# Kernel tuning notes

Measured on AMD Instinct MI355X. Metric: run time of the kernel, lower is better.

The kernel has to match this reference:

```python
import jax, jax.numpy as jnp
import numpy as np
from jax import lax

KERNEL_EPS = 1e-4   # eps in softmax_kernel
ATTN_EPS = 1e-6     # eps in causal_linear_attention
CHUNK = 64          # chunk length for the causal scan


def softmax_kernel(data, projection_matrix, is_query):
    # data: [b,h,n,d], projection_matrix: [r,d]
    d = data.shape[-1]
    r = projection_matrix.shape[0]
    data_normalizer = d ** -0.25
    ratio = r ** -0.5
    data_dash = jnp.einsum('bhnd,rd->bhnr', data_normalizer * data, projection_matrix)
    diag_data = (jnp.sum(data ** 2, axis=-1) * 0.5 * data_normalizer ** 2)[..., None]  # [b,h,n,1]
    if is_query:
        stab = jnp.max(data_dash, axis=-1, keepdims=True)
    else:
        stab = jnp.max(data_dash)
    return ratio * (jnp.exp(data_dash - diag_data - stab) + KERNEL_EPS)


def causal_linear_attention(qp, kp, v, chunk=CHUNK, eps=ATTN_EPS):
    # qp,kp: [b,h,n,r] feature maps; v: [b,h,n,e]
    b, h, n, r = qp.shape
    e = v.shape[-1]
    nc = n // chunk
    # -> [nc, b, h, chunk, *] for lax.scan over chunks
    qs = jnp.moveaxis(qp.reshape(b, h, nc, chunk, r), 2, 0)
    ks = jnp.moveaxis(kp.reshape(b, h, nc, chunk, r), 2, 0)
    vs = jnp.moveaxis(v.reshape(b, h, nc, chunk, e), 2, 0)

    def step(carry, xs):
        k_last, ctx_last = carry  # [b,h,r], [b,h,r,e]
        qch, kch, vch = xs        # [b,h,c,r], [b,h,c,r], [b,h,c,e]
        k_cum = k_last[:, :, None, :] + jnp.cumsum(kch, axis=2)              # [b,h,c,r]
        D_inv = 1.0 / jnp.einsum('bhcr,bhcr->bhc', qch, k_cum + eps)         # [b,h,c]
        ctx = jnp.einsum('bhcr,bhce->bhcre', kch, vch)                       # [b,h,c,r,e]
        ctx_cum = ctx_last[:, :, None] + jnp.cumsum(ctx, axis=2)             # [b,h,c,r,e]
        out = jnp.einsum('bhcre,bhcr,bhc->bhce', ctx_cum, qch, D_inv)        # [b,h,c,e]
        return (k_cum[:, :, -1], ctx_cum[:, :, -1]), out

    init = (jnp.zeros((b, h, r), qp.dtype), jnp.zeros((b, h, r, e), qp.dtype))
    _, outs = lax.scan(step, init, (qs, ks, vs))  # outs: [nc,b,h,c,e]
    return jnp.moveaxis(outs, 0, 2).reshape(b, h, n, e)


def setup_inputs() -> dict:
    key = jax.random.key(0)
    kq, kk, kv, kp = jax.random.split(key, 4)
    b, h, n, d, r = 2, 8, 4096, 64, 256
    q = jax.random.normal(kq, (b, h, n, d), dtype=jnp.float32)
    k = jax.random.normal(kk, (b, h, n, d), dtype=jnp.float32)
    v = jax.random.normal(kv, (b, h, n, d), dtype=jnp.float32)
    projection_matrix = jax.random.normal(kp, (r, d), dtype=jnp.float32)
    return {"q": q, "k": k, "v": v, "projection_matrix": projection_matrix}


def reference(q, k, v, projection_matrix):
    qp = softmax_kernel(q, projection_matrix, is_query=True)
    kp = softmax_kernel(k, projection_matrix, is_query=False)
    return causal_linear_attention(qp, kp, v)
```

## Files before the change

### kernel.cpp

```cpp
#include <hip/hip_runtime.h>


typedef unsigned short ushort_t;
typedef __attribute__((ext_vector_type(8))) short bf16x8;
typedef __attribute__((ext_vector_type(4))) float f32x4;

#define KEPS 1e-4f
#define AEPS 1e-6f
#define NORMIZER 0.35355339059327373f
#define RATIO 0.0625f

__device__ __forceinline__ ushort_t bf16r(float f) {
  unsigned u = __float_as_uint(f);
  return (ushort_t)((u + 0x7fffu + ((u >> 16) & 1u)) >> 16);
}
__device__ __forceinline__ float ubf(ushort_t h) {
  return __uint_as_float((unsigned)h << 16);
}

__global__ __launch_bounds__(256) void pconv_kernel(
    const float* __restrict__ P, ushort_t* __restrict__ Phi,
    ushort_t* __restrict__ Plo)
{
  int idx = blockIdx.x * 1024 + threadIdx.x;
  #pragma unroll
  for (int p = 0; p < 4; ++p) {
    int i = idx + p * 256;
    float x = P[i];
    ushort_t h = bf16r(x);
    Phi[i] = h;
    Plo[i] = bf16r(x - ubf(h));
  }
}

__global__ __launch_bounds__(256, 4) void feat_mfma(
    const float* __restrict__ Q, const float* __restrict__ K,
    const ushort_t* __restrict__ Phi, const ushort_t* __restrict__ Plo,
    ushort_t* __restrict__ qp, ushort_t* __restrict__ E,
    float* __restrict__ bmax)
{
  __shared__ union {
    struct { ushort_t Xhi[64 * 72]; ushort_t Xlo[64 * 72]; } s;
    ushort_t outb[64 * 72];
  } u;
  __shared__ ushort_t Pq[2][64 * 72];
  __shared__ float diagS[64];
  __shared__ float redm[4];

  int bid = blockIdx.x, tid = threadIdx.x;
  bool isK = bid >= 1024;
  const float* X = isK ? K : Q;
  size_t rowbase = (size_t)(isK ? bid - 1024 : bid) * 64;

  #pragma unroll
  for (int p = 0; p < 4; ++p) {
    int idx = tid + p * 256;
    int row = idx >> 4, c4 = idx & 15;
    float4 x = *(const float4*)&X[(rowbase + row) * 64 + c4 * 4];
    ushort4 h, l;
    h.x = bf16r(x.x); l.x = bf16r(x.x - ubf(h.x));
    h.y = bf16r(x.y); l.y = bf16r(x.y - ubf(h.y));
    h.z = bf16r(x.z); l.z = bf16r(x.z - ubf(h.z));
    h.w = bf16r(x.w); l.w = bf16r(x.w - ubf(h.w));
    *(ushort4*)&u.s.Xhi[row * 72 + c4 * 4] = h;
    *(ushort4*)&u.s.Xlo[row * 72 + c4 * 4] = l;
    float ss = x.x * x.x + x.y * x.y + x.z * x.z + x.w * x.w;
    ss += __shfl_xor(ss, 1, 64); ss += __shfl_xor(ss, 2, 64);
    ss += __shfl_xor(ss, 4, 64); ss += __shfl_xor(ss, 8, 64);
    if ((tid & 15) == 0) diagS[row] = 0.0625f * ss;
  }
  __syncthreads();

  int lane = tid & 63, wv = tid >> 6;
  int n15 = lane & 15, quad = lane >> 4;

  bf16x8 ah[2], al[2];
  #pragma unroll
  for (int ks = 0; ks < 2; ++ks) {
    int off = (16 * wv + n15) * 72 + quad * 8 + 32 * ks;
    ah[ks] = *(const bf16x8*)&u.s.Xhi[off];
    al[ks] = *(const bf16x8*)&u.s.Xlo[off];
  }

  f32x4 acc[16];
  #pragma unroll
  for (int tc = 0; tc < 16; ++tc) acc[tc] = f32x4{0.f, 0.f, 0.f, 0.f};

  #pragma unroll
  for (int q4 = 0; q4 < 4; ++q4) {
    if (q4) __syncthreads();
    #pragma unroll
    for (int t = 0; t < 2; ++t) {
      int f = tid + t * 256;
      int cl = f >> 3, k8 = (f & 7) * 8;
      size_t g = (size_t)(q4 * 64 + cl) * 64 + k8;
      *(bf16x8*)&Pq[0][cl * 72 + k8] = *(const bf16x8*)&Phi[g];
      *(bf16x8*)&Pq[1][cl * 72 + k8] = *(const bf16x8*)&Plo[g];
    }
    __syncthreads();
    #pragma unroll
    for (int tcl = 0; tcl < 4; ++tcl) {
      f32x4 a = acc[q4 * 4 + tcl];
      #pragma unroll
      for (int ks = 0; ks < 2; ++ks) {
        int off = (16 * tcl + n15) * 72 + quad * 8 + 32 * ks;
        bf16x8 bh = *(const bf16x8*)&Pq[0][off];
        bf16x8 bl = *(const bf16x8*)&Pq[1][off];
        a = __builtin_amdgcn_mfma_f32_16x16x32_bf16(ah[ks], bh, a, 0, 0, 0);
        a = __builtin_amdgcn_mfma_f32_16x16x32_bf16(ah[ks], bl, a, 0, 0, 0);
        a = __builtin_amdgcn_mfma_f32_16x16x32_bf16(al[ks], bh, a, 0, 0, 0);
      }
      acc[q4 * 4 + tcl] = a;
    }
  }

  float dg[4];
  #pragma unroll
  for (int r = 0; r < 4; ++r) dg[r] = diagS[16 * wv + quad * 4 + r];

  float sub[4];
  if (!isK) {
    #pragma unroll
    for (int r = 0; r < 4; ++r) {
      float mx = -3.0e38f;
      #pragma unroll
      for (int tc = 0; tc < 16; ++tc) mx = fmaxf(mx, acc[tc][r]);
      #pragma unroll
      for (int s = 1; s < 16; s <<= 1) mx = fmaxf(mx, __shfl_xor(mx, s, 64));
      sub[r] = dg[r] + NORMIZER * mx;
    }
  } else {
    float bm = -3.0e38f;
    #pragma unroll
    for (int tc = 0; tc < 16; ++tc)
      #pragma unroll
      for (int r = 0; r < 4; ++r) bm = fmaxf(bm, acc[tc][r]);
    #pragma unroll
    for (int s = 1; s < 64; s <<= 1) bm = fmaxf(bm, __shfl_xor(bm, s, 64));
    if (lane == 0) redm[wv] = bm;
    #pragma unroll
    for (int r = 0; r < 4; ++r) sub[r] = dg[r];
  }

  ushort_t* dst = (isK ? E : qp) + rowbase * 256;
  #pragma unroll
  for (int qt = 0; qt < 4; ++qt) {
    __syncthreads();
    #pragma unroll
    for (int t4 = 0; t4 < 4; ++t4) {
      int tc = qt * 4 + t4;
      #pragma unroll
      for (int r = 0; r < 4; ++r) {
        int row = 16 * wv + quad * 4 + r;
        float ex = __expf(NORMIZER * acc[tc][r] - sub[r]);
        float val = isK ? ex : RATIO * (ex + KEPS);
        u.outb[row * 72 + t4 * 16 + n15] = bf16r(val);
      }
    }
    __syncthreads();
    int row = tid >> 2, c0 = (tid & 3) * 16;
    bf16x8 v0 = *(const bf16x8*)&u.outb[row * 72 + c0];
    bf16x8 v1 = *(const bf16x8*)&u.outb[row * 72 + c0 + 8];
    *(bf16x8*)&dst[row * 256 + qt * 64 + c0] = v0;
    *(bf16x8*)&dst[row * 256 + qt * 64 + c0 + 8] = v1;
  }

  if (isK && tid == 0) {
    float m4 = fmaxf(fmaxf(redm[0], redm[1]), fmaxf(redm[2], redm[3]));
    bmax[bid - 1024] = NORMIZER * m4;
  }
}

__global__ __launch_bounds__(256) void kmax_reduce(
    const float* __restrict__ bmax, float* __restrict__ kmax)
{
  __shared__ float red[4];
  int tid = threadIdx.x;
  float m = fmaxf(fmaxf(bmax[tid], bmax[tid + 256]),
                  fmaxf(bmax[tid + 512], bmax[tid + 768]));
  #pragma unroll
  for (int s = 1; s < 64; s <<= 1) m = fmaxf(m, __shfl_xor(m, s, 64));
  if ((tid & 63) == 0) red[tid >> 6] = m;
  __syncthreads();
  if (tid == 0)
    *kmax = fmaxf(fmaxf(red[0], red[1]), fmaxf(red[2], red[3]));
}

__global__ __launch_bounds__(256) void chunksum_mfma(
    const ushort_t* __restrict__ E, const float* __restrict__ V,
    ushort_t* __restrict__ SE, float* __restrict__ zE, float* __restrict__ SV)
{
  __shared__ ushort_t Et[256 * 72];
  __shared__ ushort_t Vt[64 * 72];
  __shared__ float red2[256];

  int bc = blockIdx.x, tid = threadIdx.x;
  size_t ebase = (size_t)bc * 16384;

  #pragma unroll
  for (int p = 0; p < 8; ++p) {
    int g = (tid + p * 256) * 8;
    int pos = g >> 8, j0 = g & 255;
    bf16x8 ev = *(const bf16x8*)&E[ebase + g];
    #pragma unroll
    for (int jj = 0; jj < 8; ++jj) {
      int j = j0 + jj;
      int pr = (pos + 8 * ((j >> 3) & 7)) & 63;
      Et[j * 72 + pr] = (ushort_t)ev[jj];
    }
  }
  float vsum = 0.f;
  #pragma unroll
  for (int p = 0; p < 16; ++p) {
    int g = tid + p * 256;
    int pos = g >> 6, e = g & 63;
    float x = V[(size_t)bc * 4096 + g];
    vsum += x;
    int pr = (pos + 8 * ((e >> 3) & 7)) & 63;
    Vt[e * 72 + pr] = bf16r(x);
  }
  red2[tid] = vsum;
  __syncthreads();
  if (tid < 64)
    SV[(size_t)bc * 64 + tid] =
        red2[tid] + red2[64 + tid] + red2[128 + tid] + red2[192 + tid];

  {
    float s = 0.f;
    #pragma unroll
    for (int m8 = 0; m8 < 8; ++m8) {
      bf16x8 r8 = *(const bf16x8*)&Et[tid * 72 + m8 * 8];
      #pragma unroll
      for (int x = 0; x < 8; ++x) s += ubf((ushort_t)r8[x]);
    }
    zE[(size_t)bc * 256 + tid] = s;
  }

  int lane = tid & 63, wv = tid >> 6;
  int n15 = lane & 15, quad = lane >> 4;

  bf16x8 aV[2];
  {
    int e = 16 * wv + n15;
    int rot = 8 * ((e >> 3) & 7);
    #pragma unroll
    for (int ks = 0; ks < 2; ++ks) {
      int pr = (quad * 8 + 32 * ks + rot) & 63;
      aV[ks] = *(const bf16x8*)&Vt[e * 72 + pr];
    }
  }

  f32x4 acc[16];
  #pragma unroll
  for (int tc = 0; tc < 16; ++tc) {
    int j = 16 * tc + n15;
    int rot = 8 * ((j >> 3) & 7);
    f32x4 a = {0.f, 0.f, 0.f, 0.f};
    #pragma unroll
    for (int ks = 0; ks < 2; ++ks) {
      int pr = (quad * 8 + 32 * ks + rot) & 63;
      bf16x8 b = *(const bf16x8*)&Et[j * 72 + pr];
      a = __builtin_amdgcn_mfma_f32_16x16x32_bf16(aV[ks], b, a, 0, 0, 0);
    }
    acc[tc] = a;
  }
  __syncthreads();

  ushort_t* outS = Et;
  #pragma unroll
  for (int tc = 0; tc < 16; ++tc)
    #pragma unroll
    for (int r = 0; r < 4; ++r) {
      int e = 16 * wv + quad * 4 + r;
      outS[e * 264 + 16 * tc + n15] = bf16r(acc[tc][r]);
    }
  __syncthreads();
  #pragma unroll
  for (int p = 0; p < 8; ++p) {
    int g = (tid + p * 256) * 8;
    int e = g >> 8, j0 = g & 255;
    bf16x8 vv = *(const bf16x8*)&outS[e * 264 + j0];
    *(bf16x8*)&SE[ebase + g] = vv;
  }
}

__global__ __launch_bounds__(256) void prefix_kernel(
    ushort_t* __restrict__ S, float* __restrict__ zE,
    const float* __restrict__ SV, const float* __restrict__ kmax)
{
  int b = blockIdx.x;
  float m = *kmax;
  float c1 = RATIO * __expf(-m);
  const float c0 = RATIO * KEPS;
  if (b < 1024) {
    int flat = b * 256 + threadIdx.x;
    int bh = flat >> 14;
    int idx = flat & 16383;
    int e = idx >> 8;
    size_t base = (size_t)bh * 1048576 + idx;
    const float* svp = SV + (size_t)bh * 4096 + e;
    float runE = 0.f, runV = 0.f;
    for (int cc = 0; cc < 64; cc += 8) {
      ushort_t t[8]; float sv[8];
      #pragma unroll
      for (int u2 = 0; u2 < 8; ++u2) {
        t[u2] = S[base + (size_t)(cc + u2) * 16384];
        sv[u2] = svp[(size_t)(cc + u2) * 64];
      }
      #pragma unroll
      for (int u2 = 0; u2 < 8; ++u2) {
        S[base + (size_t)(cc + u2) * 16384] = bf16r(c1 * runE + c0 * runV);
        runE += ubf(t[u2]);
        runV += sv[u2];
      }
    }
  } else {
    int bh = b - 1024;
    int j = threadIdx.x;
    size_t base = (size_t)bh * 16384 + j;
    float run = 0.f;
    for (int cc = 0; cc < 64; cc += 8) {
      float t[8];
      #pragma unroll
      for (int u2 = 0; u2 < 8; ++u2)
        t[u2] = zE[base + (size_t)(cc + u2) * 256];
      #pragma unroll
      for (int u2 = 0; u2 < 8; ++u2) {
        zE[base + (size_t)(cc + u2) * 256] = run;
        run += c1 * t[u2] + 64.0f * c0;
      }
    }
  }
}

__global__ __launch_bounds__(256) void fused_mfma(
    const ushort_t* __restrict__ qp, const ushort_t* __restrict__ E,
    const float* __restrict__ kmax, const float* __restrict__ Z,
    const ushort_t* __restrict__ S, const float* __restrict__ V,
    float* __restrict__ out)
{
  __shared__ ushort_t As[64 * 72];
  __shared__ ushort_t Vt[64 * 72];
  __shared__ float zv[256];
  __shared__ float qsumS[64];
  __shared__ float dqS[64];

  int bc = blockIdx.x, tid = threadIdx.x;
  int lane = tid & 63, wv = tid >> 6;
  int n15 = lane & 15, quad = lane >> 4;
  float m = *kmax;
  float c1 = RATIO * __expf(-m);
  const float c0 = RATIO * KEPS;
  size_t base = (size_t)bc * 16384;

  zv[tid] = Z[(size_t)bc * 256 + tid] + AEPS;
  #pragma unroll
  for (int p = 0; p < 16; ++p) {
    int idx = tid + p * 256;
    int t = idx >> 6, e = idx & 63;
    Vt[e * 72 + t] = bf16r(V[(size_t)bc * 4096 + idx]);
  }
  __syncthreads();

  bf16x8 aQ[8];
  #pragma unroll
  for (int ks = 0; ks < 8; ++ks)
    aQ[ks] = *(const bf16x8*)&qp[base + (size_t)(16 * wv + n15) * 256 + quad * 8 + 32 * ks];

  float qsum = 0.f, dq = 0.f;
  #pragma unroll
  for (int ks = 0; ks < 8; ++ks)
    #pragma unroll
    for (int j = 0; j < 8; ++j) {
      float qv = ubf((ushort_t)aQ[ks][j]);
      qsum += qv;
      dq += qv * zv[quad * 8 + 32 * ks + j];
    }
  qsum += __shfl_xor(qsum, 16, 64); qsum += __shfl_xor(qsum, 32, 64);
  dq   += __shfl_xor(dq, 16, 64);   dq   += __shfl_xor(dq, 32, 64);
  if (quad == 0) { qsumS[16 * wv + n15] = qsum; dqS[16 * wv + n15] = dq; }

  bf16x8 bcur[8], bnxt[8];
  #pragma unroll
  for (int ks = 0; ks < 8; ++ks)
    bcur[ks] = *(const bf16x8*)&E[base + (size_t)n15 * 256 + quad * 8 + 32 * ks];

  float rs[4] = {0.f, 0.f, 0.f, 0.f};
  #pragma unroll
  for (int tc = 0; tc < 4; ++tc) {
    if (tc < 3) {
      #pragma unroll
      for (int ks = 0; ks < 8; ++ks)
        bnxt[ks] = *(const bf16x8*)&E[base + (size_t)(16 * (tc + 1) + n15) * 256 + quad * 8 + 32 * ks];
    }
    f32x4 g = {0.f, 0.f, 0.f, 0.f};
    #pragma unroll
    for (int ks = 0; ks < 8; ++ks)
      g = __builtin_amdgcn_mfma_f32_16x16x32_bf16(aQ[ks], bcur[ks], g, 0, 0, 0);
    #pragma unroll
    for (int r = 0; r < 4; ++r) {
      int i = 16 * wv + quad * 4 + r;
      int t = 16 * tc + n15;
      float val = (t <= i) ? (c1 * g[r] + c0 * qsumS[i]) : 0.f;
      As[i * 72 + t] = bf16r(val);
      rs[r] += val;
    }
    #pragma unroll
    for (int ks = 0; ks < 8; ++ks) bcur[ks] = bnxt[ks];
  }

  float dinv[4];
  #pragma unroll
  for (int r = 0; r < 4; ++r) {
    float v = rs[r];
    #pragma unroll
    for (int s = 1; s < 16; s <<= 1) v += __shfl_xor(v, s, 64);
    int i = 16 * wv + quad * 4 + r;
    dinv[r] = 1.f / (dqS[i] + v);
  }

  #pragma unroll
  for (int ks = 0; ks < 8; ++ks)
    bcur[ks] = *(const bf16x8*)&S[base + (size_t)n15 * 256 + quad * 8 + 32 * ks];

  #pragma unroll
  for (int ec = 0; ec < 4; ++ec) {
    if (ec < 3) {
      #pragma unroll
      for (int ks = 0; ks < 8; ++ks)
        bnxt[ks] = *(const bf16x8*)&S[base + (size_t)(16 * (ec + 1) + n15) * 256 + quad * 8 + 32 * ks];
    }
    f32x4 o = {0.f, 0.f, 0.f, 0.f};
    #pragma unroll
    for (int ks = 0; ks < 8; ++ks)
      o = __builtin_amdgcn_mfma_f32_16x16x32_bf16(aQ[ks], bcur[ks], o, 0, 0, 0);
    #pragma unroll
    for (int ks = 0; ks < 2; ++ks) {
      bf16x8 a2 = *(const bf16x8*)&As[(16 * wv + n15) * 72 + quad * 8 + 32 * ks];
      bf16x8 b2 = *(const bf16x8*)&Vt[(16 * ec + n15) * 72 + quad * 8 + 32 * ks];
      o = __builtin_amdgcn_mfma_f32_16x16x32_bf16(a2, b2, o, 0, 0, 0);
    }
    #pragma unroll
    for (int r = 0; r < 4; ++r) {
      int i = 16 * wv + quad * 4 + r;
      out[(size_t)bc * 4096 + (size_t)i * 64 + 16 * ec + n15] = o[r] * dinv[r];
    }
    #pragma unroll
    for (int ks = 0; ks < 8; ++ks) bcur[ks] = bnxt[ks];
  }
}

extern "C" void kernel_launch(void* const* d_in, const int* in_sizes, int n_in,
                              void* d_out, int out_size, void* d_ws, size_t ws_size,
                              hipStream_t stream)
{
  const float* q = (const float*)d_in[0];
  const float* k = (const float*)d_in[1];
  const float* v = (const float*)d_in[2];
  const float* P = (const float*)d_in[3];
  float* out = (float*)d_out;

  ushort_t* qp  = (ushort_t*)d_ws;
  ushort_t* E   = qp + 16777216;
  ushort_t* S   = E + 16777216;
  float*    zE  = (float*)(S + 16777216);
  float*    SV  = zE + 262144;
  ushort_t* Phi = (ushort_t*)(SV + 65536);
  ushort_t* Plo = Phi + 16384;
  float*    bmax = (float*)(Plo + 16384);
  float*    kmax = bmax + 1024;

  pconv_kernel<<<16, 256, 0, stream>>>(P, Phi, Plo);
  feat_mfma<<<2048, 256, 0, stream>>>(q, k, Phi, Plo, qp, E, bmax);
  kmax_reduce<<<1, 256, 0, stream>>>(bmax, kmax);
  chunksum_mfma<<<1024, 256, 0, stream>>>(E, v, S, zE, SV);
  prefix_kernel<<<1040, 256, 0, stream>>>(S, zE, SV, kmax);
  fused_mfma<<<1024, 256, 0, stream>>>(qp, E, kmax, zE, S, v, out);
}
```

Baseline: 185.3 us.

## Stage E/S tiles into swizzled LDS via async global_load_lds double buffering

In the fused chunk kernel, each wave used to load the shared E and S tiles straight from global memory into registers, so all four waves read the same data separately. Now each 16-row tile is loaded once per block with global_load_lds into a double-buffered LDS area, using an XOR swizzle to avoid bank conflicts. The E and S phases are merged into one 8-step loop that prefetches the next tile while the current one runs through MFMA. This cuts redundant global traffic and register pressure, but adds a barrier and vmcnt wait every step.

```diff
diff --git a/kernel.cpp b/kernel.cpp
--- a/kernel.cpp
+++ b/kernel.cpp
@@ -333,6 +333,20 @@
   }
 }
 
+__device__ __forceinline__ void stage_tile(const ushort_t* __restrict__ gt,
+                                           ushort_t* lds0, int tid, int wv) {
+  #pragma unroll
+  for (int i = 0; i < 2; ++i) {
+    int D = i * 256 + tid;
+    int row = D >> 5, cl = D & 31;
+    int sc = (row << 5) | (cl ^ (row & 7));
+    __builtin_amdgcn_global_load_lds(
+        (const __attribute__((address_space(1))) void*)(gt + sc * 8),
+        (__attribute__((address_space(3))) void*)(lds0 + (i * 256 + wv * 64) * 8),
+        16, 0, 0);
+  }
+}
+
 __global__ __launch_bounds__(256) void fused_mfma(
     const ushort_t* __restrict__ qp, const ushort_t* __restrict__ E,
     const float* __restrict__ kmax, const float* __restrict__ Z,
@@ -341,6 +355,7 @@
 {
   __shared__ ushort_t As[64 * 72];
   __shared__ ushort_t Vt[64 * 72];
+  __shared__ ushort_t Bst[2][4096];
   __shared__ float zv[256];
   __shared__ float qsumS[64];
   __shared__ float dqS[64];
@@ -362,6 +377,8 @@
   }
   __syncthreads();
 
+  stage_tile(E + base, &Bst[0][0], tid, wv);
+
   bf16x8 aQ[8];
   #pragma unroll
   for (int ks = 0; ks < 8; ++ks)
@@ -380,73 +397,65 @@
   dq   += __shfl_xor(dq, 16, 64);   dq   += __shfl_xor(dq, 32, 64);
   if (quad == 0) { qsumS[16 * wv + n15] = qsum; dqS[16 * wv + n15] = dq; }
 
-  bf16x8 bcur[8], bnxt[8];
-  #pragma unroll
-  for (int ks = 0; ks < 8; ++ks)
-    bcur[ks] = *(const bf16x8*)&E[base + (size_t)n15 * 256 + quad * 8 + 32 * ks];
-
   float rs[4] = {0.f, 0.f, 0.f, 0.f};
-  #pragma unroll
-  for (int tc = 0; tc < 4; ++tc) {
-    if (tc < 3) {
-      #pragma unroll
-      for (int ks = 0; ks < 8; ++ks)
-        bnxt[ks] = *(const bf16x8*)&E[base + (size_t)(16 * (tc + 1) + n15) * 256 + quad * 8 + 32 * ks];
+  float dinv[4] = {0.f, 0.f, 0.f, 0.f};
+
+  #pragma unroll
+  for (int t = 0; t < 8; ++t) {
+    asm volatile("s_waitcnt vmcnt(0)" ::: "memory");
+    __builtin_amdgcn_s_barrier();
+    if (t < 7) {
+      const ushort_t* gt = (t < 3) ? (E + base + (size_t)(t + 1) * 4096)
+                                   : (S + base + (size_t)(t - 3) * 4096);
+      stage_tile(gt, &Bst[(t + 1) & 1][0], tid, wv);
+    }
+
+    bf16x8 bf[8];
+    #pragma unroll
+    for (int ks = 0; ks < 8; ++ks) {
+      int rc = (4 * ks + quad) ^ (n15 & 7);
+      bf[ks] = *(const bf16x8*)&Bst[t & 1][(n15 * 32 + rc) * 8];
     }
     f32x4 g = {0.f, 0.f, 0.f, 0.f};
     #pragma unroll
     for (int ks = 0; ks < 8; ++ks)
-      g = __builtin_amdgcn_mfma_f32_16x16x32_bf16(aQ[ks], bcur[ks], g, 0, 0, 0);
-    #pragma unroll
-    for (int r = 0; r < 4; ++r) {
-      int i = 16 * wv + quad * 4 + r;
-      int t = 16 * tc + n15;
-      float val = (t <= i) ? (c1 * g[r] + c0 * qsumS[i]) : 0.f;
-      As[i * 72 + t] = bf16r(val);
-      rs[r] += val;
-    }
-    #pragma unroll
-    for (int ks = 0; ks < 8; ++ks) bcur[ks] = bnxt[ks];
-  }
-
-  float dinv[4];
-  #pragma unroll
-  for (int r = 0; r < 4; ++r) {
-    float v = rs[r];
-    #pragma unroll
-    for (int s = 1; s < 16; s <<= 1) v += __shfl_xor(v, s, 64);
-    int i = 16 * wv + quad * 4 + r;
-    dinv[r] = 1.f / (dqS[i] + v);
-  }
-
-  #pragma unroll
-  for (int ks = 0; ks < 8; ++ks)
-    bcur[ks] = *(const bf16x8*)&S[base + (size_t)n15 * 256 + quad * 8 + 32 * ks];
-
-  #pragma unroll
-  for (int ec = 0; ec < 4; ++ec) {
-    if (ec < 3) {
-      #pragma unroll
-      for (int ks = 0; ks < 8; ++ks)
-        bnxt[ks] = *(const bf16x8*)&S[base + (size_t)(16 * (ec + 1) + n15) * 256 + quad * 8 + 32 * ks];
-    }
-    f32x4 o = {0.f, 0.f, 0.f, 0.f};
-    #pragma unroll
-    for (int ks = 0; ks < 8; ++ks)
-      o = __builtin_amdgcn_mfma_f32_16x16x32_bf16(aQ[ks], bcur[ks], o, 0, 0, 0);
-    #pragma unroll
-    for (int ks = 0; ks < 2; ++ks) {
-      bf16x8 a2 = *(const bf16x8*)&As[(16 * wv + n15) * 72 + quad * 8 + 32 * ks];
-      bf16x8 b2 = *(const bf16x8*)&Vt[(16 * ec + n15) * 72 + quad * 8 + 32 * ks];
-      o = __builtin_amdgcn_mfma_f32_16x16x32_bf16(a2, b2, o, 0, 0, 0);
-    }
-    #pragma unroll
-    for (int r = 0; r < 4; ++r) {
-      int i = 16 * wv + quad * 4 + r;
-      out[(size_t)bc * 4096 + (size_t)i * 64 + 16 * ec + n15] = o[r] * dinv[r];
-    }
-    #pragma unroll
-    for (int ks = 0; ks < 8; ++ks) bcur[ks] = bnxt[ks];
+      g = __builtin_amdgcn_mfma_f32_16x16x32_bf16(aQ[ks], bf[ks], g, 0, 0, 0);
+
+    if (t < 4) {
+      int tc = t;
+      #pragma unroll
+      for (int r = 0; r < 4; ++r) {
+        int i = 16 * wv + quad * 4 + r;
+        int tt = 16 * tc + n15;
+        float val = (tt <= i) ? (c1 * g[r] + c0 * qsumS[i]) : 0.f;
+        As[i * 72 + tt] = bf16r(val);
+        rs[r] += val;
+      }
+      if (t == 3) {
+        #pragma unroll
+        for (int r = 0; r < 4; ++r) {
+          float v2 = rs[r];
+          #pragma unroll
+          for (int s = 1; s < 16; s <<= 1) v2 += __shfl_xor(v2, s, 64);
+          int i = 16 * wv + quad * 4 + r;
+          dinv[r] = 1.f / (dqS[i] + v2);
+        }
+      }
+    } else {
+      int ec = t - 4;
+      f32x4 o = g;
+      #pragma unroll
+      for (int ks = 0; ks < 2; ++ks) {
+        bf16x8 a2 = *(const bf16x8*)&As[(16 * wv + n15) * 72 + quad * 8 + 32 * ks];
+        bf16x8 b2 = *(const bf16x8*)&Vt[(16 * ec + n15) * 72 + quad * 8 + 32 * ks];
+        o = __builtin_amdgcn_mfma_f32_16x16x32_bf16(a2, b2, o, 0, 0, 0);
+      }
+      #pragma unroll
+      for (int r = 0; r < 4; ++r) {
+        int i = 16 * wv + quad * 4 + r;
+        out[(size_t)bc * 4096 + (size_t)i * 64 + 16 * ec + n15] = o[r] * dinv[r];
+      }
+    }
   }
 }
 
```

Result: faster. 168.8 us (-8.9%).
